# Kernel tuning notes

Measured on AMD Instinct MI355X. Metric: run time of the kernel, lower is better.

## Reference

```python
import math
import jax, jax.numpy as jnp
import numpy as np

B, S, D = 1, 2048, 4096
H, KVH, HD = 32, 8, 128  # head_dim = D // H; n_rep = H // KVH = 4
MAXB, MAXS = 1, 2048
ROPE_THETA = 10000.0


def setup_inputs() -> dict:
    key = jax.random.key(0)
    ks = jax.random.split(key, 6)
    x = jax.random.normal(ks[0], (B, S, D), dtype=jnp.float32)
    sc = 0.02
    wq = jax.random.normal(ks[1], (D, H * HD), dtype=jnp.float32) * sc
    wk = jax.random.normal(ks[2], (D, KVH * HD), dtype=jnp.float32) * sc
    wv = jax.random.normal(ks[3], (D, KVH * HD), dtype=jnp.float32) * sc
    wo = jax.random.normal(ks[4], (H * HD, D), dtype=jnp.float32) * sc
    # rotary phases: freqs_cis[t, j] = exp(i * t * theta^(-2j/hd))
    inv_freq = 1.0 / (ROPE_THETA ** (jnp.arange(0, HD, 2, dtype=jnp.float32) / HD))
    ang = jnp.arange(S, dtype=jnp.float32)[:, None] * inv_freq[None, :]  # [S, HD//2]
    freqs_cos = jnp.cos(ang)
    freqs_sin = jnp.sin(ang)
    # causal additive mask over the cache window (start_pos=0 prefill)
    mask = jnp.where(jnp.triu(jnp.ones((S, S), dtype=bool), k=1), -1e9, 0.0).astype(jnp.float32)
    cache_k = jnp.zeros((MAXB, MAXS, KVH, HD), dtype=jnp.float32)
    cache_v = jnp.zeros((MAXB, MAXS, KVH, HD), dtype=jnp.float32)
    return {"x": x, "wq": wq, "wk": wk, "wv": wv, "wo": wo,
            "freqs_cos": freqs_cos, "freqs_sin": freqs_sin, "mask": mask,
            "cache_k": cache_k, "cache_v": cache_v, "start_pos": 0}


def _apply_rope(t, cos, sin):
    # t: [B, S, h, HD]; cos/sin: [S, HD//2]
    te, to = t[..., ::2], t[..., 1::2]
    cos = cos[None, :, None, :]
    sin = sin[None, :, None, :]
    out = jnp.stack([te * cos - to * sin, to * cos + te * sin], axis=-1)
    return out.reshape(t.shape)


def _repeat_kv(t, n_rep):
    # faithful to source: rep axis inserted before kv-head axis
    bs, slen, n_kv, hd = t.shape
    if n_rep == 1:
        return t
    return jnp.repeat(t[:, :, None, :, :], n_rep, axis=2).reshape(bs, slen, n_kv * n_rep, hd)


def reference(x, wq, wk, wv, wo, freqs_cos, freqs_sin, mask, cache_k, cache_v, start_pos):
    bsz, seqlen, _ = x.shape
    n_rep = H // KVH
    xq = (x @ wq).reshape(bsz, seqlen, H, HD)
    xk = (x @ wk).reshape(bsz, seqlen, KVH, HD)
    xv = (x @ wv).reshape(bsz, seqlen, KVH, HD)
    xq = _apply_rope(xq, freqs_cos, freqs_sin)
    xk = _apply_rope(xk, freqs_cos, freqs_sin)
    # KV-cache append
    cache_k = cache_k.at[:bsz, start_pos:start_pos + seqlen].set(xk)
    cache_v = cache_v.at[:bsz, start_pos:start_pos + seqlen].set(xv)
    keys = _repeat_kv(cache_k[:bsz, :start_pos + seqlen], n_rep)    # [B, T, H, HD]
    values = _repeat_kv(cache_v[:bsz, :start_pos + seqlen], n_rep)  # [B, T, H, HD]
    scores = jnp.einsum('bqhd,bkhd->bhqk', xq, keys) / math.sqrt(HD)
    scores = scores + mask[None, None, :, :]
    probs = jax.nn.softmax(scores, axis=-1)
    out = jnp.einsum('bhqk,bkhd->bqhd', probs, values).reshape(bsz, seqlen, H * HD)
    return out @ wo
```

## Files before the change

kernel.cpp:

```cpp
#include <hip/hip_runtime.h>
#include <stdint.h>


using bf16x8 = __attribute__((ext_vector_type(8))) short;
using f32x4  = __attribute__((ext_vector_type(4))) float;
using s16x4  = __attribute__((ext_vector_type(4))) short;

__device__ __forceinline__ short f2bf(float f) {
    union { float f; unsigned u; } v; v.f = f;
    unsigned r = v.u + 0x7fffu + ((v.u >> 16) & 1u);
    return (short)(r >> 16);
}
__device__ __forceinline__ float bf2f(short s) {
    union { unsigned u; float f; } v; v.u = ((unsigned)(unsigned short)s) << 16;
    return v.f;
}

#define GLL16(gp, lp)                                                          \
    __builtin_amdgcn_global_load_lds(                                          \
        (const __attribute__((address_space(1))) void*)(gp),                   \
        (__attribute__((address_space(3))) void*)(lp), 16, 0, 0)

__global__ __launch_bounds__(256) void cvt_f32_bf16(const float* __restrict__ x,
                                                    short* __restrict__ y, int n) {
    int i = (blockIdx.x * 256 + threadIdx.x) * 4;
    if (i >= n) return;
    f32x4 v = *(const f32x4*)(x + i);
    s16x4 o;
    o.x = f2bf(v.x); o.y = f2bf(v.y); o.z = f2bf(v.z); o.w = f2bf(v.w);
    *(s16x4*)(y + i) = o;
}

__global__ __launch_bounds__(256) void transpose_f32_bf16(const float* __restrict__ W,
                                                          short* __restrict__ WT,
                                                          int K, int N) {
    __shared__ float t[32][33];
    int n0 = blockIdx.x * 32, k0 = blockIdx.y * 32;
    int tx = threadIdx.x, ty = threadIdx.y;
#pragma unroll
    for (int i = 0; i < 32; i += 8)
        t[ty + i][tx] = W[(size_t)(k0 + ty + i) * N + n0 + tx];
    __syncthreads();
#pragma unroll
    for (int i = 0; i < 32; i += 8)
        WT[(size_t)(n0 + ty + i) * K + k0 + tx] = f2bf(t[tx][ty + i]);
}

__global__ __launch_bounds__(256) void transpose_bf16(const short* __restrict__ A,
                                                      short* __restrict__ AT,
                                                      int R, int C, int lda) {
    __shared__ short t[32][33];
    int c0 = blockIdx.x * 32, r0 = blockIdx.y * 32;
    int tx = threadIdx.x, ty = threadIdx.y;
#pragma unroll
    for (int i = 0; i < 32; i += 8)
        t[ty + i][tx] = A[(size_t)(r0 + ty + i) * lda + c0 + tx];
    __syncthreads();
#pragma unroll
    for (int i = 0; i < 32; i += 8)
        AT[(size_t)(c0 + ty + i) * R + r0 + tx] = t[tx][ty + i];
}

__global__ __launch_bounds__(256) void gemm_bf16(const short* __restrict__ A,
                                                 const short* __restrict__ BT,
                                                 float* __restrict__ Cf,
                                                 short* __restrict__ Cb,
                                                 short* __restrict__ Cb2,
                                                 int M, int N, int K,
                                                 int split, int ld1, int ld2) {
    __shared__ short As[128 * 32];
    __shared__ short Bs[128 * 32];
    const int tid  = threadIdx.x;
    const int wave = tid >> 6, lane = tid & 63;
    const int lrow = lane & 15, quad = lane >> 4, lk8 = quad * 8;
    const int bm = blockIdx.y * 128, bn = blockIdx.x * 128;
    const int wm = (wave >> 1) * 64, wn = (wave & 1) * 64;

    f32x4 acc[4][4];
#pragma unroll
    for (int i = 0; i < 4; i++)
#pragma unroll
        for (int j = 0; j < 4; j++) acc[i][j] = (f32x4){0.f, 0.f, 0.f, 0.f};

    for (int k0 = 0; k0 < K; k0 += 32) {
        __syncthreads();
#pragma unroll
        for (int s = 0; s < 2; s++) {
            int idx = tid * 8 + s * 2048;
            int row = idx >> 5, col = idx & 31;
            GLL16(A  + (size_t)(bm + row) * K + k0 + col, &As[idx]);
            GLL16(BT + (size_t)(bn + row) * K + k0 + col, &Bs[idx]);
        }
        __syncthreads();
        bf16x8 af[4], bfr[4];
#pragma unroll
        for (int i = 0; i < 4; i++) af[i]  = *(const bf16x8*)&As[(wm + i * 16 + lrow) * 32 + lk8];
#pragma unroll
        for (int j = 0; j < 4; j++) bfr[j] = *(const bf16x8*)&Bs[(wn + j * 16 + lrow) * 32 + lk8];
#pragma unroll
        for (int i = 0; i < 4; i++)
#pragma unroll
            for (int j = 0; j < 4; j++)
                acc[i][j] = __builtin_amdgcn_mfma_f32_16x16x32_bf16(af[i], bfr[j], acc[i][j], 0, 0, 0);
    }

    short* Co;
    int ldc, ncol0;
    if (bn < split) { Co = Cb;  ldc = ld1; ncol0 = 0;     }
    else            { Co = Cb2; ldc = ld2; ncol0 = split; }

#pragma unroll
    for (int i = 0; i < 4; i++)
#pragma unroll
        for (int j = 0; j < 4; j++)
#pragma unroll
            for (int r = 0; r < 4; r++) {
                int m = bm + wm + i * 16 + quad * 4 + r;
                int n = bn + wn + j * 16 + lrow;
                float v = acc[i][j][r];
                if (Cf) Cf[(size_t)m * N + n] = v;
                else    Co[(size_t)m * ldc + (n - ncol0)] = f2bf(v);
            }
}

__global__ __launch_bounds__(256) void rope_kernel(short* __restrict__ q,
                                                   short* __restrict__ kv,
                                                   const float* __restrict__ fc,
                                                   const float* __restrict__ fs) {
    int s = blockIdx.x, t = threadIdx.x;
#pragma unroll
    for (int p = t; p < 2048; p += 256) {
        int i = p & 63;
        float c = fc[s * 64 + i], sn = fs[s * 64 + i];
        int base = s * 4096 + 2 * p;
        float e = bf2f(q[base]), o = bf2f(q[base + 1]);
        q[base]     = f2bf(e * c - o * sn);
        q[base + 1] = f2bf(o * c + e * sn);
    }
#pragma unroll
    for (int p = t; p < 512; p += 256) {
        int i = p & 63;
        float c = fc[s * 64 + i], sn = fs[s * 64 + i];
        int base = s * 2048 + 2 * p;
        float e = bf2f(kv[base]), o = bf2f(kv[base + 1]);
        kv[base]     = f2bf(e * c - o * sn);
        kv[base + 1] = f2bf(o * c + e * sn);
    }
}

#define KSLD 136
#define VSLD 40
__global__ __launch_bounds__(256) void attn_kernel(const short* __restrict__ Q,
                                                   const short* __restrict__ KV,
                                                   const short* __restrict__ VT,
                                                   short* __restrict__ AO) {
    const int qb = 63 - blockIdx.x;
    const int kvh = blockIdx.y;
    const int wave = threadIdx.x >> 6, lane = threadIdx.x & 63;
    const int lrow = lane & 15, quad = lane >> 4, lk8 = quad * 8;
    const int h = wave * 8 + kvh;
    const int q0 = qb * 32;

    __shared__ short Ks[32 * KSLD];
    __shared__ short Vs[128 * VSLD];
    __shared__ short Pw[4][2][16 * 32];

    bf16x8 aq[2][4];
#pragma unroll
    for (int rs = 0; rs < 2; rs++) {
        const short* qrow = Q + (size_t)(q0 + rs * 16 + lrow) * 4096 + h * 128;
#pragma unroll
        for (int f = 0; f < 4; f++) aq[rs][f] = *(const bf16x8*)(qrow + f * 32 + lk8);
    }

    f32x4 o_acc[2][8];
#pragma unroll
    for (int rs = 0; rs < 2; rs++)
#pragma unroll
        for (int d = 0; d < 8; d++) o_acc[rs][d] = (f32x4){0.f, 0.f, 0.f, 0.f};
    float l_part[2][4];
#pragma unroll
    for (int rs = 0; rs < 2; rs++)
#pragma unroll
        for (int r = 0; r < 4; r++) l_part[rs][r] = 0.f;

    const int nkt = qb + 1;
    const float sc = 0.08838834764831845f;

    for (int kt = 0; kt < nkt; kt++) {
        __syncthreads();
#pragma unroll
        for (int c = 0; c < 2; c++) {
            int idx = (threadIdx.x + c * 256) * 8;
            int key = idx >> 7, d = idx & 127;
            *(bf16x8*)&Ks[key * KSLD + d] =
                *(const bf16x8*)(KV + (size_t)(kt * 32 + key) * 2048 + kvh * 128 + d);
            int dr = idx >> 5, kc = idx & 31;
            *(bf16x8*)&Vs[dr * VSLD + kc] =
                *(const bf16x8*)(VT + (size_t)(kvh * 128 + dr) * 2048 + kt * 32 + kc);
        }
        __syncthreads();

        f32x4 s0[2], s1[2];
#pragma unroll
        for (int rs = 0; rs < 2; rs++) { s0[rs] = (f32x4){0.f,0.f,0.f,0.f}; s1[rs] = s0[rs]; }
#pragma unroll
        for (int f = 0; f < 4; f++) {
            bf16x8 b0 = *(const bf16x8*)&Ks[(lrow)      * KSLD + f * 32 + lk8];
            bf16x8 b1 = *(const bf16x8*)&Ks[(16 + lrow) * KSLD + f * 32 + lk8];
#pragma unroll
            for (int rs = 0; rs < 2; rs++) {
                s0[rs] = __builtin_amdgcn_mfma_f32_16x16x32_bf16(aq[rs][f], b0, s0[rs], 0, 0, 0);
                s1[rs] = __builtin_amdgcn_mfma_f32_16x16x32_bf16(aq[rs][f], b1, s1[rs], 0, 0, 0);
            }
        }

        int keyg0 = kt * 32 + lrow, keyg1 = keyg0 + 16;
#pragma unroll
        for (int rs = 0; rs < 2; rs++)
#pragma unroll
            for (int r = 0; r < 4; r++) {
                int qg = q0 + rs * 16 + quad * 4 + r;
                float p0 = (keyg0 > qg) ? 0.f : __expf(s0[rs][r] * sc);
                float p1 = (keyg1 > qg) ? 0.f : __expf(s1[rs][r] * sc);
                l_part[rs][r] += p0 + p1;
                Pw[wave][rs][(quad * 4 + r) * 32 + lrow]      = f2bf(p0);
                Pw[wave][rs][(quad * 4 + r) * 32 + 16 + lrow] = f2bf(p1);
            }

#pragma unroll
        for (int rs = 0; rs < 2; rs++) {
            bf16x8 ap = *(const bf16x8*)&Pw[wave][rs][lrow * 32 + lk8];
#pragma unroll
            for (int dt = 0; dt < 8; dt++) {
                bf16x8 bv = *(const bf16x8*)&Vs[(dt * 16 + lrow) * VSLD + lk8];
                o_acc[rs][dt] = __builtin_amdgcn_mfma_f32_16x16x32_bf16(ap, bv, o_acc[rs][dt], 0, 0, 0);
            }
        }
    }

#pragma unroll
    for (int rs = 0; rs < 2; rs++)
#pragma unroll
        for (int r = 0; r < 4; r++) {
            float l = l_part[rs][r];
#pragma unroll
            for (int off = 1; off < 16; off <<= 1) l += __shfl_xor(l, off, 64);
            float inv = 1.f / l;
#pragma unroll
            for (int dt = 0; dt < 8; dt++) {
                int qg = q0 + rs * 16 + quad * 4 + r;
                AO[(size_t)qg * 4096 + h * 128 + dt * 16 + lrow] =
                    f2bf(o_acc[rs][dt][r] * inv);
            }
        }
}

extern "C" void kernel_launch(void* const* d_in, const int* in_sizes, int n_in,
                              void* d_out, int out_size, void* d_ws, size_t ws_size,
                              hipStream_t stream) {
    (void)in_sizes; (void)n_in; (void)out_size; (void)ws_size;
    const float* x  = (const float*)d_in[0];
    const float* wq = (const float*)d_in[1];
    const float* wk = (const float*)d_in[2];
    const float* wv = (const float*)d_in[3];
    const float* wo = (const float*)d_in[4];
    const float* fc = (const float*)d_in[5];
    const float* fs = (const float*)d_in[6];
    float* out = (float*)d_out;

    char* ws = (char*)d_ws;
    size_t off = 0;
    auto carve = [&](size_t bytes) { char* p = ws + off; off = (off + bytes + 255) & ~(size_t)255; return p; };
    short* xb     = (short*)carve(2048u * 4096u * 2);
    short* wqkvT  = (short*)carve(6144u * 4096u * 2);
    short* woT    = (short*)carve(4096u * 4096u * 2);
    short* qb     = (short*)carve(2048u * 4096u * 2);
    short* kvb    = (short*)carve(2048u * 2048u * 2);
    short* vtb    = (short*)carve(1024u * 2048u * 2);
    short* aob    = xb;

    dim3 tb(32, 8);
    cvt_f32_bf16<<<8192, 256, 0, stream>>>(x, xb, 2048 * 4096);
    transpose_f32_bf16<<<dim3(128, 128), tb, 0, stream>>>(wq, wqkvT, 4096, 4096);
    transpose_f32_bf16<<<dim3(32, 128),  tb, 0, stream>>>(wk, wqkvT + (size_t)4096 * 4096, 4096, 1024);
    transpose_f32_bf16<<<dim3(32, 128),  tb, 0, stream>>>(wv, wqkvT + (size_t)5120 * 4096, 4096, 1024);
    transpose_f32_bf16<<<dim3(128, 128), tb, 0, stream>>>(wo, woT, 4096, 4096);

    gemm_bf16<<<dim3(48, 16), 256, 0, stream>>>(xb, wqkvT, nullptr, qb, kvb,
                                                2048, 6144, 4096, 4096, 4096, 2048);

    rope_kernel<<<2048, 256, 0, stream>>>(qb, kvb, fc, fs);
    transpose_bf16<<<dim3(32, 64), tb, 0, stream>>>(kvb + 1024, vtb, 2048, 1024, 2048);

    attn_kernel<<<dim3(64, 8), 256, 0, stream>>>(qb, kvb, vtb, aob);

    gemm_bf16<<<dim3(32, 16), 256, 0, stream>>>(aob, woT, out, nullptr, nullptr,
                                                2048, 4096, 4096, 4096, 4096, 4096);
}
```

Before: 606.8 us.

## Fuse RoPE into QKV GEMM epilogue, prefetch 64-key attention tiles, merge transposes

The attention kernel now processes 64-key tiles and loads the next K/V tile into registers while the current one computes, which halves the number of barrier round-trips and overlaps global loads with MFMA work. It also raises wave priority around the MFMA sections. RoPE moves into the QKV GEMM epilogue using a lane-pair shuffle, which removes a separate read-modify-write pass over q and k. The four weight transposes merge into one launch. The cost is higher register and LDS use in attention and some extra masked work on the diagonal tile.

```diff
diff --git a/kernel.cpp b/kernel.cpp
--- a/kernel.cpp
+++ b/kernel.cpp
@@ -31,11 +31,21 @@
     *(s16x4*)(y + i) = o;
 }
 
-__global__ __launch_bounds__(256) void transpose_f32_bf16(const float* __restrict__ W,
-                                                          short* __restrict__ WT,
-                                                          int K, int N) {
+__global__ __launch_bounds__(256) void transpose_w4(const float* __restrict__ wq,
+                                                    const float* __restrict__ wk,
+                                                    const float* __restrict__ wv,
+                                                    const float* __restrict__ wo,
+                                                    short* __restrict__ wqkvT,
+                                                    short* __restrict__ woT) {
     __shared__ float t[32][33];
-    int n0 = blockIdx.x * 32, k0 = blockIdx.y * 32;
+    int bx = blockIdx.x;
+    int by = blockIdx.y;
+    const float* W; short* WT; int N;
+    if (by < 128)      { W = wq; WT = wqkvT;                         N = 4096; }
+    else if (by < 160) { W = wk; WT = wqkvT + (size_t)4096 * 4096;   N = 1024; by -= 128; }
+    else if (by < 192) { W = wv; WT = wqkvT + (size_t)5120 * 4096;   N = 1024; by -= 160; }
+    else               { W = wo; WT = woT;                           N = 4096; by -= 192; }
+    int n0 = by * 32, k0 = bx * 32;
     int tx = threadIdx.x, ty = threadIdx.y;
 #pragma unroll
     for (int i = 0; i < 32; i += 8)
@@ -43,7 +53,7 @@
     __syncthreads();
 #pragma unroll
     for (int i = 0; i < 32; i += 8)
-        WT[(size_t)(n0 + ty + i) * K + k0 + tx] = f2bf(t[tx][ty + i]);
+        WT[(size_t)(n0 + ty + i) * 4096 + k0 + tx] = f2bf(t[tx][ty + i]);
 }
 
 __global__ __launch_bounds__(256) void transpose_bf16(const short* __restrict__ A,
@@ -67,7 +77,10 @@
                                                  short* __restrict__ Cb,
                                                  short* __restrict__ Cb2,
                                                  int M, int N, int K,
-                                                 int split, int ld1, int ld2) {
+                                                 int split, int ld1, int ld2,
+                                                 int ropeN,
+                                                 const float* __restrict__ fc,
+                                                 const float* __restrict__ fs) {
     __shared__ short As[128 * 32];
     __shared__ short Bs[128 * 32];
     const int tid  = threadIdx.x;
@@ -112,58 +125,43 @@
 #pragma unroll
     for (int i = 0; i < 4; i++)
 #pragma unroll
-        for (int j = 0; j < 4; j++)
+        for (int j = 0; j < 4; j++) {
+            int nn = bn + wn + j * 16 + lrow;
+            bool dorope = (nn < ropeN);
 #pragma unroll
             for (int r = 0; r < 4; r++) {
                 int m = bm + wm + i * 16 + quad * 4 + r;
-                int n = bn + wn + j * 16 + lrow;
                 float v = acc[i][j][r];
-                if (Cf) Cf[(size_t)m * N + n] = v;
-                else    Co[(size_t)m * ldc + (n - ncol0)] = f2bf(v);
-            }
-}
-
-__global__ __launch_bounds__(256) void rope_kernel(short* __restrict__ q,
-                                                   short* __restrict__ kv,
-                                                   const float* __restrict__ fc,
-                                                   const float* __restrict__ fs) {
-    int s = blockIdx.x, t = threadIdx.x;
-#pragma unroll
-    for (int p = t; p < 2048; p += 256) {
-        int i = p & 63;
-        float c = fc[s * 64 + i], sn = fs[s * 64 + i];
-        int base = s * 4096 + 2 * p;
-        float e = bf2f(q[base]), o = bf2f(q[base + 1]);
-        q[base]     = f2bf(e * c - o * sn);
-        q[base + 1] = f2bf(o * c + e * sn);
-    }
-#pragma unroll
-    for (int p = t; p < 512; p += 256) {
-        int i = p & 63;
-        float c = fc[s * 64 + i], sn = fs[s * 64 + i];
-        int base = s * 2048 + 2 * p;
-        float e = bf2f(kv[base]), o = bf2f(kv[base + 1]);
-        kv[base]     = f2bf(e * c - o * sn);
-        kv[base + 1] = f2bf(o * c + e * sn);
-    }
+                if (dorope) {
+                    float vp = __shfl_xor(v, 1);
+                    int ip = (nn & 127) >> 1;
+                    float c = fc[m * 64 + ip], s = fs[m * 64 + ip];
+                    v = (lane & 1) ? (v * c + vp * s) : (v * c - vp * s);
+                }
+                if (Cf) Cf[(size_t)m * N + nn] = v;
+                else    Co[(size_t)m * ldc + (nn - ncol0)] = f2bf(v);
+            }
+        }
 }
 
 #define KSLD 136
-#define VSLD 40
+#define VSLD 72
+#define PSLD 72
 __global__ __launch_bounds__(256) void attn_kernel(const short* __restrict__ Q,
                                                    const short* __restrict__ KV,
                                                    const short* __restrict__ VT,
                                                    short* __restrict__ AO) {
     const int qb = 63 - blockIdx.x;
     const int kvh = blockIdx.y;
-    const int wave = threadIdx.x >> 6, lane = threadIdx.x & 63;
+    const int tid = threadIdx.x;
+    const int wave = tid >> 6, lane = tid & 63;
     const int lrow = lane & 15, quad = lane >> 4, lk8 = quad * 8;
     const int h = wave * 8 + kvh;
     const int q0 = qb * 32;
 
-    __shared__ short Ks[32 * KSLD];
+    __shared__ short Ks[64 * KSLD];
     __shared__ short Vs[128 * VSLD];
-    __shared__ short Pw[4][2][16 * 32];
+    __shared__ short Pw[4][2][16 * PSLD];
 
     bf16x8 aq[2][4];
 #pragma unroll
@@ -184,59 +182,95 @@
 #pragma unroll
         for (int r = 0; r < 4; r++) l_part[rs][r] = 0.f;
 
-    const int nkt = qb + 1;
+    const int nkt = (qb + 2) >> 1;
     const float sc = 0.08838834764831845f;
 
+    {
+        bf16x8 rK[4], rV[4];
+#pragma unroll
+        for (int c = 0; c < 4; c++) {
+            int idx = (tid + c * 256) * 8;
+            rK[c] = *(const bf16x8*)(KV + (size_t)(idx >> 7) * 2048 + kvh * 128 + (idx & 127));
+            rV[c] = *(const bf16x8*)(VT + (size_t)(kvh * 128 + (idx >> 6)) * 2048 + (idx & 63));
+        }
+#pragma unroll
+        for (int c = 0; c < 4; c++) {
+            int idx = (tid + c * 256) * 8;
+            *(bf16x8*)&Ks[(idx >> 7) * KSLD + (idx & 127)] = rK[c];
+            *(bf16x8*)&Vs[(idx >> 6) * VSLD + (idx & 63)] = rV[c];
+        }
+    }
+    __syncthreads();
+
     for (int kt = 0; kt < nkt; kt++) {
+        bf16x8 rK[4], rV[4];
+        const bool pf = (kt + 1 < nkt);
+        if (pf) {
+#pragma unroll
+            for (int c = 0; c < 4; c++) {
+                int idx = (tid + c * 256) * 8;
+                rK[c] = *(const bf16x8*)(KV + (size_t)((kt + 1) * 64 + (idx >> 7)) * 2048 + kvh * 128 + (idx & 127));
+                rV[c] = *(const bf16x8*)(VT + (size_t)(kvh * 128 + (idx >> 6)) * 2048 + (kt + 1) * 64 + (idx & 63));
+            }
+        }
+
+        f32x4 sg[2][4];
+#pragma unroll
+        for (int rs = 0; rs < 2; rs++)
+#pragma unroll
+            for (int kg = 0; kg < 4; kg++) sg[rs][kg] = (f32x4){0.f, 0.f, 0.f, 0.f};
+        __builtin_amdgcn_s_setprio(1);
+#pragma unroll
+        for (int f = 0; f < 4; f++) {
+#pragma unroll
+            for (int kg = 0; kg < 4; kg++) {
+                bf16x8 bk = *(const bf16x8*)&Ks[(kg * 16 + lrow) * KSLD + f * 32 + lk8];
+#pragma unroll
+                for (int rs = 0; rs < 2; rs++)
+                    sg[rs][kg] = __builtin_amdgcn_mfma_f32_16x16x32_bf16(aq[rs][f], bk, sg[rs][kg], 0, 0, 0);
+            }
+        }
+        __builtin_amdgcn_s_setprio(0);
+
+#pragma unroll
+        for (int rs = 0; rs < 2; rs++)
+#pragma unroll
+            for (int kg = 0; kg < 4; kg++) {
+                int keyg = kt * 64 + kg * 16 + lrow;
+#pragma unroll
+                for (int r = 0; r < 4; r++) {
+                    int qg = q0 + rs * 16 + quad * 4 + r;
+                    float p = (keyg > qg) ? 0.f : __expf(sg[rs][kg][r] * sc);
+                    l_part[rs][r] += p;
+                    Pw[wave][rs][(quad * 4 + r) * PSLD + kg * 16 + lrow] = f2bf(p);
+                }
+            }
+
+        __builtin_amdgcn_s_setprio(1);
+#pragma unroll
+        for (int rs = 0; rs < 2; rs++) {
+            bf16x8 ap0 = *(const bf16x8*)&Pw[wave][rs][lrow * PSLD + lk8];
+            bf16x8 ap1 = *(const bf16x8*)&Pw[wave][rs][lrow * PSLD + 32 + lk8];
+#pragma unroll
+            for (int dt = 0; dt < 8; dt++) {
+                bf16x8 bv0 = *(const bf16x8*)&Vs[(dt * 16 + lrow) * VSLD + lk8];
+                bf16x8 bv1 = *(const bf16x8*)&Vs[(dt * 16 + lrow) * VSLD + 32 + lk8];
+                o_acc[rs][dt] = __builtin_amdgcn_mfma_f32_16x16x32_bf16(ap0, bv0, o_acc[rs][dt], 0, 0, 0);
+                o_acc[rs][dt] = __builtin_amdgcn_mfma_f32_16x16x32_bf16(ap1, bv1, o_acc[rs][dt], 0, 0, 0);
+            }
+        }
+        __builtin_amdgcn_s_setprio(0);
+
         __syncthreads();
-#pragma unroll
-        for (int c = 0; c < 2; c++) {
-            int idx = (threadIdx.x + c * 256) * 8;
-            int key = idx >> 7, d = idx & 127;
-            *(bf16x8*)&Ks[key * KSLD + d] =
-                *(const bf16x8*)(KV + (size_t)(kt * 32 + key) * 2048 + kvh * 128 + d);
-            int dr = idx >> 5, kc = idx & 31;
-            *(bf16x8*)&Vs[dr * VSLD + kc] =
-                *(const bf16x8*)(VT + (size_t)(kvh * 128 + dr) * 2048 + kt * 32 + kc);
+        if (pf) {
+#pragma unroll
+            for (int c = 0; c < 4; c++) {
+                int idx = (tid + c * 256) * 8;
+                *(bf16x8*)&Ks[(idx >> 7) * KSLD + (idx & 127)] = rK[c];
+                *(bf16x8*)&Vs[(idx >> 6) * VSLD + (idx & 63)] = rV[c];
+            }
         }
         __syncthreads();
-
-        f32x4 s0[2], s1[2];
-#pragma unroll
-        for (int rs = 0; rs < 2; rs++) { s0[rs] = (f32x4){0.f,0.f,0.f,0.f}; s1[rs] = s0[rs]; }
-#pragma unroll
-        for (int f = 0; f < 4; f++) {
-            bf16x8 b0 = *(const bf16x8*)&Ks[(lrow)      * KSLD + f * 32 + lk8];
-            bf16x8 b1 = *(const bf16x8*)&Ks[(16 + lrow) * KSLD + f * 32 + lk8];
-#pragma unroll
-            for (int rs = 0; rs < 2; rs++) {
-                s0[rs] = __builtin_amdgcn_mfma_f32_16x16x32_bf16(aq[rs][f], b0, s0[rs], 0, 0, 0);
-                s1[rs] = __builtin_amdgcn_mfma_f32_16x16x32_bf16(aq[rs][f], b1, s1[rs], 0, 0, 0);
-            }
-        }
-
-        int keyg0 = kt * 32 + lrow, keyg1 = keyg0 + 16;
-#pragma unroll
-        for (int rs = 0; rs < 2; rs++)
-#pragma unroll
-            for (int r = 0; r < 4; r++) {
-                int qg = q0 + rs * 16 + quad * 4 + r;
-                float p0 = (keyg0 > qg) ? 0.f : __expf(s0[rs][r] * sc);
-                float p1 = (keyg1 > qg) ? 0.f : __expf(s1[rs][r] * sc);
-                l_part[rs][r] += p0 + p1;
-                Pw[wave][rs][(quad * 4 + r) * 32 + lrow]      = f2bf(p0);
-                Pw[wave][rs][(quad * 4 + r) * 32 + 16 + lrow] = f2bf(p1);
-            }
-
-#pragma unroll
-        for (int rs = 0; rs < 2; rs++) {
-            bf16x8 ap = *(const bf16x8*)&Pw[wave][rs][lrow * 32 + lk8];
-#pragma unroll
-            for (int dt = 0; dt < 8; dt++) {
-                bf16x8 bv = *(const bf16x8*)&Vs[(dt * 16 + lrow) * VSLD + lk8];
-                o_acc[rs][dt] = __builtin_amdgcn_mfma_f32_16x16x32_bf16(ap, bv, o_acc[rs][dt], 0, 0, 0);
-            }
-        }
     }
 
 #pragma unroll
@@ -282,19 +316,17 @@
 
     dim3 tb(32, 8);
     cvt_f32_bf16<<<8192, 256, 0, stream>>>(x, xb, 2048 * 4096);
-    transpose_f32_bf16<<<dim3(128, 128), tb, 0, stream>>>(wq, wqkvT, 4096, 4096);
-    transpose_f32_bf16<<<dim3(32, 128),  tb, 0, stream>>>(wk, wqkvT + (size_t)4096 * 4096, 4096, 1024);
-    transpose_f32_bf16<<<dim3(32, 128),  tb, 0, stream>>>(wv, wqkvT + (size_t)5120 * 4096, 4096, 1024);
-    transpose_f32_bf16<<<dim3(128, 128), tb, 0, stream>>>(wo, woT, 4096, 4096);
+    transpose_w4<<<dim3(128, 320), tb, 0, stream>>>(wq, wk, wv, wo, wqkvT, woT);
 
     gemm_bf16<<<dim3(48, 16), 256, 0, stream>>>(xb, wqkvT, nullptr, qb, kvb,
-                                                2048, 6144, 4096, 4096, 4096, 2048);
-
-    rope_kernel<<<2048, 256, 0, stream>>>(qb, kvb, fc, fs);
+                                                2048, 6144, 4096, 4096, 4096, 2048,
+                                                5120, fc, fs);
+
     transpose_bf16<<<dim3(32, 64), tb, 0, stream>>>(kvb + 1024, vtb, 2048, 1024, 2048);
 
     attn_kernel<<<dim3(64, 8), 256, 0, stream>>>(qb, kvb, vtb, aob);
 
     gemm_bf16<<<dim3(32, 16), 256, 0, stream>>>(aob, woT, out, nullptr, nullptr,
-                                                2048, 4096, 4096, 4096, 4096, 4096);
-}
+                                                2048, 4096, 4096, 4096, 4096, 4096,
+                                                0, fc, fs);
+}
```

New measurement: 663.1 us. 1.09x slower.
